# Kernel optimization log

Hardware: AMD Instinct MI355X
Metric: run time of the kernel (lower is better)

The kernel has to match this reference:

```python
import jax, jax.numpy as jnp
import numpy as np

T, B, F = 160, 640, 40          # time-major input [T, B, F]
H, PJ, L = 768, 256, 3          # nb_hidden, nb_proj, nb_layers
FORGET_BIAS = 1.0               # TF LSTMCell default


def _glorot(k, shape):
    std = (2.0 / (shape[0] + shape[1])) ** 0.5
    return jax.random.normal(k, shape, jnp.float32) * std


def setup_inputs() -> dict:
    key = jax.random.key(0)
    ks = jax.random.split(key, 7)
    x = jax.random.normal(ks[0], (T, B, F), jnp.float32)
    # layer 0: input dim F + proj state PJ; layers 1,2: input dim PJ + PJ
    W0 = _glorot(ks[1], (F + PJ, 4 * H)); b0 = jnp.zeros((4 * H,), jnp.float32)
    P0 = _glorot(ks[2], (H, PJ))
    W1 = _glorot(ks[3], (PJ + PJ, 4 * H)); b1 = jnp.zeros((4 * H,), jnp.float32)
    P1 = _glorot(ks[4], (H, PJ))
    W2 = _glorot(ks[5], (PJ + PJ, 4 * H)); b2 = jnp.zeros((4 * H,), jnp.float32)
    P2 = _glorot(ks[6], (H, PJ))
    return {"x": x, "W0": W0, "b0": b0, "P0": P0,
            "W1": W1, "b1": b1, "P1": P1,
            "W2": W2, "b2": b2, "P2": P2}


def _cell(xt, c, h, W, b, P):
    # TF LSTMCell with num_proj: gates on [x, m_prev]; gate order i, j, f, o.
    z = jnp.concatenate([xt, h], axis=-1) @ W + b            # [B, 4H]
    i, j, f, o = jnp.split(z, 4, axis=-1)
    c_new = jax.nn.sigmoid(f + FORGET_BIAS) * c + jax.nn.sigmoid(i) * jnp.tanh(j)
    m = jax.nn.sigmoid(o) * jnp.tanh(c_new)                  # [B, H]
    h_new = m @ P                                            # projected state [B, PJ]
    return c_new, h_new


def reference(x, W0, b0, P0, W1, b1, P1, W2, b2, P2):
    params = ((W0, b0, P0), (W1, b1, P1), (W2, b2, P2))
    Bd = x.shape[1]
    init = tuple((jnp.zeros((Bd, H), x.dtype), jnp.zeros((Bd, PJ), x.dtype))
                 for _ in range(L))

    def step(carry, xt):
        inp = xt
        new = []
        for (c, h), (W, b, P) in zip(carry, params):
            c, h = _cell(inp, c, h, W, b, P)
            new.append((c, h))
            inp = h
        return tuple(new), None

    carry, _ = jax.lax.scan(step, init, x)
    emb = carry[-1][1]                                       # last layer h at final step, [B, PJ]
    # tf.nn.l2_normalize
    return emb / jnp.sqrt(jnp.maximum(jnp.sum(emb * emb, axis=-1, keepdims=True), 1e-12))
```

## Files before the change

kernel.cpp:

```cpp
#include <hip/hip_runtime.h>

#define Bdim 640
#define Hdim 768
#define PJdim 256
#define Tdim 160
#define NSTEP (Tdim + 2)

typedef _Float16 half8 __attribute__((ext_vector_type(8)));
typedef float floatx4 __attribute__((ext_vector_type(4)));

constexpr size_t HB_HALFS = 3ull * Bdim * PJdim;
constexpr size_t ZP_OFF   = HB_HALFS * 2;
constexpr size_t MB_OFF   = ZP_OFF + 256;
constexpr size_t MB_HALFS = 3ull * Bdim * Hdim;
constexpr size_t X_OFF    = MB_OFF + MB_HALFS * 2;
constexpr size_t X_HALFS  = (size_t)Tdim * Bdim * 40;
constexpr size_t W_OFF    = X_OFF + X_HALFS * 2;
constexpr size_t W_HALFS  = 36ull * 131072;
constexpr size_t P_OFF    = W_OFF + W_HALFS * 2;
constexpr size_t P_HALFS  = 3ull * 196608;
constexpr size_t C_OFF    = P_OFF + P_HALFS * 2;
constexpr size_t C_BYTES  = 3ull * Bdim * Hdim * 4;

__device__ __forceinline__ float sigm(float v) { return 1.0f / (1.0f + __expf(-v)); }
__device__ __forceinline__ float tanh_fast(float v) { return 2.0f / (1.0f + __expf(-2.0f * v)) - 1.0f; }

__device__ __forceinline__ void pipe_wait(unsigned* c0, unsigned t0, unsigned* c1, unsigned t1)
{
    if (threadIdx.x == 0) {
        if (t0)
            while (__hip_atomic_load(c0, __ATOMIC_RELAXED, __HIP_MEMORY_SCOPE_AGENT) < t0)
                __builtin_amdgcn_s_sleep(1);
        if (c1 && t1)
            while (__hip_atomic_load(c1, __ATOMIC_RELAXED, __HIP_MEMORY_SCOPE_AGENT) < t1)
                __builtin_amdgcn_s_sleep(1);
        __threadfence();
    }
    __syncthreads();
}

__device__ __forceinline__ void pipe_sig(unsigned* c)
{
    __syncthreads();
    if (threadIdx.x == 0) {
        __threadfence();
        __hip_atomic_fetch_add(c, 1u, __ATOMIC_RELAXED, __HIP_MEMORY_SCOPE_AGENT);
    }
}

__global__ void repack_kernel(const float* __restrict__ x,
                              const float* __restrict__ W0, const float* __restrict__ W1,
                              const float* __restrict__ W2, const float* __restrict__ P0,
                              const float* __restrict__ P1, const float* __restrict__ P2,
                              _Float16* __restrict__ Wfrag, _Float16* __restrict__ Pfrag,
                              _Float16* __restrict__ x16)
{
    size_t idx = (size_t)blockIdx.x * 256 + threadIdx.x;
    if (idx < W_HALFS) {
        int slab = (int)(idx >> 17);
        int l = slab / 12, ht = slab % 12;
        int r  = (int)(idx & 131071);
        int kc = r >> 13;
        int r2 = r & 8191;
        int g  = r2 >> 11;
        int cf = (r2 >> 9) & 3;
        int u  = r2 & 511;
        int lane = u >> 3, e = u & 7;
        int qd = lane >> 4, ln = lane & 15;
        int k   = kc * 32 + qd * 8 + e;
        int col = g * Hdim + ht * 64 + cf * 16 + ln;
        float v;
        if (l == 0)      v = (k < 296) ? W0[(size_t)k * 3072 + col] : 0.0f;
        else if (l == 1) v = W1[(size_t)k * 3072 + col];
        else             v = W2[(size_t)k * 3072 + col];
        Wfrag[idx] = (_Float16)v;
    } else if (idx < W_HALFS + P_HALFS) {
        size_t i = idx - W_HALFS;
        int l = (int)(i / 196608);
        int r = (int)(i % 196608);
        int cq = r / 49152;
        int r2 = r % 49152;
        int kc = r2 / 2048;
        int r3 = r2 & 2047;
        int cgr = r3 >> 9;
        int u  = r3 & 511;
        int lane = u >> 3, e = u & 7;
        int qd = lane >> 4, ln = lane & 15;
        int k  = kc * 32 + qd * 8 + e;
        int pj = cq * 64 + cgr * 16 + ln;
        const float* P = (l == 0) ? P0 : (l == 1) ? P1 : P2;
        Pfrag[i] = (_Float16)P[(size_t)k * PJdim + pj];
    } else if (idx < W_HALFS + P_HALFS + X_HALFS) {
        size_t i = idx - W_HALFS - P_HALFS;
        x16[i] = (_Float16)x[i];
    }
}

__device__ __forceinline__ void gate_step(
    int l, int b0r, int h0, int KC, int t,
    const half8 (&Breg)[16][2], float (&c)[8][2],
    const float (&bia)[2], const float (&bja)[2], const float (&bfa)[2], const float (&boa)[2],
    const _Float16* __restrict__ x16, const _Float16* __restrict__ h16,
    const _Float16* __restrict__ zerop, _Float16* __restrict__ mbuf,
    _Float16* __restrict__ Ast, float* __restrict__ zst, int tid)
{
    const int wv = tid >> 6, lane = tid & 63, qd = lane >> 4, ln = lane & 15;
    const int g = wv >> 1, hh = wv & 1;
    const int qd8 = qd * 8;
    const int rowg = b0r + wv * 16 + ln;

    const _Float16* xt  = x16 + ((size_t)t * Bdim + rowg) * 40;
    const _Float16* h0b = h16 + (size_t)rowg * PJdim - 40;
    const _Float16* lob = (l > 0) ? h16 + ((size_t)(l - 1) * Bdim + rowg) * PJdim : nullptr;
    const _Float16* hib = h16 + ((size_t)l * Bdim + rowg) * PJdim - 256;

    auto srcp = [&](int kc) -> const _Float16* {
        int k = kc * 32 + qd8;
        if (l == 0) return (k < 40) ? xt + k : (k < 296) ? h0b + k : zerop;
        return (k < 256) ? lob + k : hib + k;
    };

    floatx4 acc[8][2];
    const floatx4 fz = {0.f, 0.f, 0.f, 0.f};
#pragma unroll
    for (int i = 0; i < 8; ++i) { acc[i][0] = fz; acc[i][1] = fz; }

    const int CH = KC >> 1;
    uint4 pre0 = *(const uint4*)srcp(0);
    uint4 pre1 = *(const uint4*)srcp(1);
#pragma unroll
    for (int ch = 0; ch < 8; ++ch) {
        if (ch < CH) {
            _Float16* Aw = Ast + (size_t)(ch & 1) * 8192 + wv * 512 + lane * 8;
            *(uint4*)Aw          = pre0;
            *(uint4*)(Aw + 4096) = pre1;
            if (ch + 1 < CH) {
                pre0 = *(const uint4*)srcp(2 * ch + 2);
                pre1 = *(const uint4*)srcp(2 * ch + 3);
            }
            __syncthreads();
            const _Float16* Ab = Ast + (size_t)(ch & 1) * 8192;
#pragma unroll
            for (int sub = 0; sub < 2; ++sub)
#pragma unroll
                for (int rf = 0; rf < 8; ++rf) {
                    half8 af = *(const half8*)(Ab + sub * 4096 + rf * 512 + lane * 8);
                    acc[rf][0] = __builtin_amdgcn_mfma_f32_16x16x32_f16(af, Breg[2 * ch + sub][0], acc[rf][0], 0, 0, 0);
                    acc[rf][1] = __builtin_amdgcn_mfma_f32_16x16x32_f16(af, Breg[2 * ch + sub][1], acc[rf][1], 0, 0, 0);
                }
        }
    }

    const int trow = tid >> 5;
    const int hc0  = (tid * 2) & 63;
#pragma unroll
    for (int rf = 0; rf < 8; ++rf) {
        __syncthreads();
#pragma unroll
        for (int cf = 0; cf < 2; ++cf)
#pragma unroll
            for (int r = 0; r < 4; ++r)
                zst[(qd * 4 + r) * 256 + g * 64 + hh * 32 + cf * 16 + ln] = acc[rf][cf][r];
        __syncthreads();
        _Float16 mh[2];
#pragma unroll
        for (int j = 0; j < 2; ++j) {
            int hc = hc0 + j;
            float zi = zst[trow * 256 + hc]       + bia[j];
            float zj = zst[trow * 256 + 64 + hc]  + bja[j];
            float zf = zst[trow * 256 + 128 + hc] + bfa[j];
            float zo = zst[trow * 256 + 192 + hc] + boa[j];
            float cn = sigm(zf) * c[rf][j] + sigm(zi) * tanh_fast(zj);
            c[rf][j] = cn;
            mh[j] = (_Float16)(sigm(zo) * tanh_fast(cn));
        }
        union { _Float16 h2[2]; unsigned u; } pk;
        pk.h2[0] = mh[0]; pk.h2[1] = mh[1];
        int row_g = b0r + rf * 16 + trow;
        *(unsigned*)(mbuf + ((size_t)l * Bdim + row_g) * Hdim + h0 + hc0) = pk.u;
    }
}

__device__ __forceinline__ void proj_step(
    int l, int b0r, int cq, const half8 (&Preg)[24],
    const _Float16* __restrict__ mbuf, _Float16* __restrict__ h16,
    _Float16* __restrict__ Ast, int tid)
{
    const int wv = tid >> 6, lane = tid & 63, qd = lane >> 4, ln = lane & 15;
    const int rh = wv >> 2, cgi = wv & 3;
    const int rowg = b0r + wv * 16 + ln;
    const _Float16* mrow = mbuf + ((size_t)l * Bdim + rowg) * Hdim + qd * 8;

    floatx4 pacc[4];
    const floatx4 fz = {0.f, 0.f, 0.f, 0.f};
#pragma unroll
    for (int i = 0; i < 4; ++i) pacc[i] = fz;

    uint4 pre0 = *(const uint4*)(mrow);
    uint4 pre1 = *(const uint4*)(mrow + 32);
#pragma unroll
    for (int ch = 0; ch < 12; ++ch) {
        _Float16* Aw = Ast + (size_t)(ch & 1) * 8192 + wv * 512 + lane * 8;
        *(uint4*)Aw          = pre0;
        *(uint4*)(Aw + 4096) = pre1;
        if (ch < 11) {
            pre0 = *(const uint4*)(mrow + (2 * ch + 2) * 32);
            pre1 = *(const uint4*)(mrow + (2 * ch + 3) * 32);
        }
        __syncthreads();
        const _Float16* Ab = Ast + (size_t)(ch & 1) * 8192;
#pragma unroll
        for (int sub = 0; sub < 2; ++sub)
#pragma unroll
            for (int rfl = 0; rfl < 4; ++rfl) {
                half8 af = *(const half8*)(Ab + sub * 4096 + (rh * 4 + rfl) * 512 + lane * 8);
                pacc[rfl] = __builtin_amdgcn_mfma_f32_16x16x32_f16(af, Preg[2 * ch + sub], pacc[rfl], 0, 0, 0);
            }
    }
#pragma unroll
    for (int rfl = 0; rfl < 4; ++rfl)
#pragma unroll
        for (int r = 0; r < 4; ++r) {
            int row = b0r + (rh * 4 + rfl) * 16 + qd * 4 + r;
            h16[((size_t)l * Bdim + row) * PJdim + cq * 64 + cgi * 16 + ln] = (_Float16)pacc[rfl][r];
        }
}

__device__ __forceinline__ void load_Breg(const _Float16* __restrict__ Wfrag, int l, int ht,
                                          int wv, int lane, half8 (&Breg)[16][2])
{
    const int g = wv >> 1, hh = wv & 1;
    const _Float16* wslab = Wfrag + ((size_t)(l * 12 + ht)) * 131072;
#pragma unroll
    for (int kc = 0; kc < 16; ++kc)
#pragma unroll
        for (int cf = 0; cf < 2; ++cf)
            Breg[kc][cf] = *(const half8*)(wslab + kc * 8192 + g * 2048 + (hh * 2 + cf) * 512 + lane * 8);
}

__device__ __forceinline__ void load_Preg(const _Float16* __restrict__ Pfrag, int l, int cq,
                                          int wv, int lane, half8 (&Preg)[24])
{
    const int cgi = wv & 3;
    const _Float16* pslab = Pfrag + (size_t)l * 196608 + (size_t)cq * 49152;
#pragma unroll
    for (int kc = 0; kc < 24; ++kc)
        Preg[kc] = *(const half8*)(pslab + kc * 2048 + cgi * 512 + lane * 8);
}

__device__ __forceinline__ void load_bias(const float* __restrict__ bias, int h0, int tid,
                                          float (&bia)[2], float (&bja)[2], float (&bfa)[2], float (&boa)[2])
{
    int hcg = h0 + ((tid * 2) & 63);
#pragma unroll
    for (int j = 0; j < 2; ++j) {
        bia[j] = bias[hcg + j];
        bja[j] = bias[Hdim + hcg + j];
        bfa[j] = bias[2 * Hdim + hcg + j] + 1.0f;
        boa[j] = bias[3 * Hdim + hcg + j];
    }
}

__device__ __forceinline__ void finalize_row(const _Float16* __restrict__ h16,
                                             float* __restrict__ out, int row, int lane)
{
    const _Float16* e = h16 + ((size_t)2 * Bdim + row) * PJdim + lane * 4;
    float v0 = (float)e[0], v1 = (float)e[1], v2 = (float)e[2], v3 = (float)e[3];
    float ss = v0 * v0 + v1 * v1 + v2 * v2 + v3 * v3;
#pragma unroll
    for (int o = 32; o > 0; o >>= 1) ss += __shfl_xor(ss, o, 64);
    float rs = rsqrtf(fmaxf(ss, 1e-12f));
    float4 o4; o4.x = v0 * rs; o4.y = v1 * rs; o4.z = v2 * rs; o4.w = v3 * rs;
    *(float4*)(out + (size_t)row * PJdim + lane * 4) = o4;
}

__global__ __launch_bounds__(512)
void lstm_persist(const _Float16* __restrict__ x16, const _Float16* __restrict__ Wfrag,
                  const _Float16* __restrict__ Pfrag,
                  const float* __restrict__ bias0, const float* __restrict__ bias1,
                  const float* __restrict__ bias2,
                  _Float16* __restrict__ h16, _Float16* __restrict__ mbuf,
                  const _Float16* __restrict__ zerop, float* __restrict__ out,
                  unsigned* __restrict__ flags)
{
    __shared__ __align__(16) _Float16 Ast[2 * 8192];
    __shared__ __align__(16) float zst[16 * 256];

    const int tid = threadIdx.x, bid = blockIdx.x;
    const int wv = tid >> 6, lane = tid & 63;

    const int xcd = bid & 7, slot = bid >> 3;
    const int gid = xcd * 2 + (slot >> 4);
    const int rr  = slot & 15;
    if (gid >= 15) return;
    const int bt2 = gid / 3, l = gid % 3;
    const int b0r = bt2 * 128;

    unsigned* gd = flags + (size_t)gid * 64;
    unsigned* pd = gd + 32;

    if (rr < 12) {
        const int ht = rr, h0 = ht * 64;
        const int KC = (l == 0) ? 10 : 16;
        half8 Breg[16][2];
        load_Breg(Wfrag, l, ht, wv, lane, Breg);
        float bia[2], bja[2], bfa[2], boa[2];
        load_bias((l == 0) ? bias0 : (l == 1) ? bias1 : bias2, h0, tid, bia, bja, bfa, boa);
        float c[8][2];
#pragma unroll
        for (int i = 0; i < 8; ++i) { c[i][0] = 0.f; c[i][1] = 0.f; }
        unsigned* pd_lo = (l > 0) ? flags + (size_t)(gid - 1) * 64 + 32 : nullptr;
        for (int t = 0; t < Tdim; ++t) {
            pipe_wait(pd, 4u * (unsigned)t, pd_lo, (l > 0) ? 4u * (unsigned)(t + 1) : 0u);
            gate_step(l, b0r, h0, KC, t, Breg, c, bia, bja, bfa, boa,
                      x16, h16, zerop, mbuf, Ast, zst, tid);
            pipe_sig(gd);
        }
        if (l == 2 && rr < 8) {
            pipe_wait(pd, 4u * (unsigned)Tdim, nullptr, 0u);
            int row0 = b0r + rr * 16 + wv * 2;
            finalize_row(h16, out, row0, lane);
            finalize_row(h16, out, row0 + 1, lane);
        }
    } else {
        const int cq = rr - 12;
        half8 Preg[24];
        load_Preg(Pfrag, l, cq, wv, lane, Preg);
        unsigned* gd_hi = (l < 2) ? flags + (size_t)(gid + 1) * 64 : nullptr;
        for (int t = 0; t < Tdim; ++t) {
            pipe_wait(gd, 12u * (unsigned)(t + 1), gd_hi, (l < 2) ? 12u * (unsigned)t : 0u);
            proj_step(l, b0r, cq, Preg, mbuf, h16, Ast, tid);
            pipe_sig(pd);
        }
    }
}

__global__ __launch_bounds__(512)
void gate_fb(const _Float16* __restrict__ x16, const _Float16* __restrict__ Wfrag,
             const float* __restrict__ bias0, const float* __restrict__ bias1,
             const float* __restrict__ bias2,
             _Float16* __restrict__ h16, _Float16* __restrict__ mbuf,
             const _Float16* __restrict__ zerop, float* __restrict__ cfb, int s)
{
    __shared__ __align__(16) _Float16 Ast[2 * 8192];
    __shared__ __align__(16) float zst[16 * 256];
    const int tid = threadIdx.x, bid = blockIdx.x;
    const int ht = bid % 12, z = bid / 12, l = z % 3, bt2 = z / 3;
    const int t = s - l;
    if (t < 0 || t >= Tdim) return;
    const int wv = tid >> 6, lane = tid & 63;
    const int b0r = bt2 * 128, h0 = ht * 64;
    const int KC = (l == 0) ? 10 : 16;
    half8 Breg[16][2];
    load_Breg(Wfrag, l, ht, wv, lane, Breg);
    float bia[2], bja[2], bfa[2], boa[2];
    load_bias((l == 0) ? bias0 : (l == 1) ? bias1 : bias2, h0, tid, bia, bja, bfa, boa);
    const int trow = tid >> 5, hc0 = (tid * 2) & 63;
    float c[8][2];
#pragma unroll
    for (int rf = 0; rf < 8; ++rf)
#pragma unroll
        for (int j = 0; j < 2; ++j)
            c[rf][j] = cfb[((size_t)l * Bdim + b0r + rf * 16 + trow) * Hdim + h0 + hc0 + j];
    gate_step(l, b0r, h0, KC, t, Breg, c, bia, bja, bfa, boa, x16, h16, zerop, mbuf, Ast, zst, tid);
#pragma unroll
    for (int rf = 0; rf < 8; ++rf)
#pragma unroll
        for (int j = 0; j < 2; ++j)
            cfb[((size_t)l * Bdim + b0r + rf * 16 + trow) * Hdim + h0 + hc0 + j] = c[rf][j];
}

__global__ __launch_bounds__(512)
void proj_fb(const _Float16* __restrict__ Pfrag, const _Float16* __restrict__ mbuf,
             _Float16* __restrict__ h16, int s)
{
    __shared__ __align__(16) _Float16 Ast[2 * 8192];
    const int tid = threadIdx.x, bid = blockIdx.x;
    const int cq = bid & 3, z = bid >> 2, l = z % 3, bt2 = z / 3;
    const int tp = s - l;
    if (tp < 0 || tp >= Tdim) return;
    const int wv = tid >> 6, lane = tid & 63;
    half8 Preg[24];
    load_Preg(Pfrag, l, cq, wv, lane, Preg);
    proj_step(l, bt2 * 128, cq, Preg, mbuf, h16, Ast, tid);
}

__global__ __launch_bounds__(512)
void fin_fb(const _Float16* __restrict__ h16, float* __restrict__ out)
{
    int row = blockIdx.x * 8 + (threadIdx.x >> 6);
    finalize_row(h16, out, row, threadIdx.x & 63);
}

extern "C" void kernel_launch(void* const* d_in, const int* in_sizes, int n_in,
                              void* d_out, int out_size, void* d_ws, size_t ws_size,
                              hipStream_t stream)
{
    (void)in_sizes; (void)n_in; (void)out_size; (void)ws_size;
    const float* x  = (const float*)d_in[0];
    const float* W0 = (const float*)d_in[1];
    const float* b0 = (const float*)d_in[2];
    const float* P0 = (const float*)d_in[3];
    const float* W1 = (const float*)d_in[4];
    const float* b1 = (const float*)d_in[5];
    const float* P1 = (const float*)d_in[6];
    const float* W2 = (const float*)d_in[7];
    const float* b2 = (const float*)d_in[8];
    const float* P2 = (const float*)d_in[9];

    char* ws = (char*)d_ws;
    _Float16* h16   = (_Float16*)(ws);
    _Float16* zerop = (_Float16*)(ws + ZP_OFF);
    _Float16* mbuf  = (_Float16*)(ws + MB_OFF);
    _Float16* x16   = (_Float16*)(ws + X_OFF);
    _Float16* Wfrag = (_Float16*)(ws + W_OFF);
    _Float16* Pfrag = (_Float16*)(ws + P_OFF);
    float*    cfb   = (float*)(ws + C_OFF);
    unsigned* flags = (unsigned*)(ws + C_OFF);
    float*    outp  = (float*)d_out;

    hipMemsetAsync(ws, 0, ZP_OFF + 256, stream);
    hipMemsetAsync(cfb, 0, C_BYTES, stream);

    {
        constexpr size_t total = W_HALFS + P_HALFS + X_HALFS;
        int grid = (int)((total + 255) / 256);
        repack_kernel<<<grid, 256, 0, stream>>>(x, W0, W1, W2, P0, P1, P2, Wfrag, Pfrag, x16);
    }

    int occ = 0;
    hipError_t oe = hipOccupancyMaxActiveBlocksPerMultiprocessor(&occ, lstm_persist, 512, 0);
    bool coop = (oe == hipSuccess && occ >= 1);
    if (coop) {
        void* args[] = { (void*)&x16, (void*)&Wfrag, (void*)&Pfrag,
                         (void*)&b0, (void*)&b1, (void*)&b2,
                         (void*)&h16, (void*)&mbuf, (void*)&zerop, (void*)&outp,
                         (void*)&flags };
        hipError_t le = hipLaunchCooperativeKernel((const void*)lstm_persist,
                                                   dim3(256), dim3(512), args, 0, stream);
        if (le != hipSuccess) { (void)hipGetLastError(); coop = false; }
    }
    if (!coop) {
        for (int s = 0; s < NSTEP; ++s) {
            gate_fb<<<180, 512, 0, stream>>>(x16, Wfrag, b0, b1, b2, h16, mbuf, zerop, cfb, s);
            proj_fb<<<60, 512, 0, stream>>>(Pfrag, mbuf, h16, s);
        }
        fin_fb<<<80, 512, 0, stream>>>(h16, outp);
    }
}
```

Measured before the change: 4.839 ms.

## Replace inter-block threadfences with relaxed agent-scope coherent loads and stores

Removes the __threadfence calls from the pipeline wait and signal helpers. All cross-block shared data (h16, mbuf, and the final embedding) is now read and written through relaxed agent-scope atomic loads and stores so that it bypasses non-coherent caches. Launch bounds are also raised to request two blocks per CU. Without fences, the relaxed ordering between the data stores and the flag increment may not guarantee visibility, and the 64-bit split loads and 16-bit atomic stores may be slower than the wide vector accesses they replace.

```diff
diff --git a/kernel.cpp b/kernel.cpp
--- a/kernel.cpp
+++ b/kernel.cpp
@@ -25,6 +25,25 @@
 __device__ __forceinline__ float sigm(float v) { return 1.0f / (1.0f + __expf(-v)); }
 __device__ __forceinline__ float tanh_fast(float v) { return 2.0f / (1.0f + __expf(-2.0f * v)) - 1.0f; }
 
+__device__ __forceinline__ uint4 ld_coh16(const void* p) {
+    const unsigned long long* q = (const unsigned long long*)p;
+    unsigned long long a = __hip_atomic_load(q,     __ATOMIC_RELAXED, __HIP_MEMORY_SCOPE_AGENT);
+    unsigned long long b = __hip_atomic_load(q + 1, __ATOMIC_RELAXED, __HIP_MEMORY_SCOPE_AGENT);
+    uint4 r; r.x = (unsigned)a; r.y = (unsigned)(a >> 32);
+    r.z = (unsigned)b; r.w = (unsigned)(b >> 32);
+    return r;
+}
+__device__ __forceinline__ unsigned long long ld_coh8(const void* p) {
+    return __hip_atomic_load((const unsigned long long*)p, __ATOMIC_RELAXED, __HIP_MEMORY_SCOPE_AGENT);
+}
+__device__ __forceinline__ void st_coh32(void* p, unsigned v) {
+    __hip_atomic_store((unsigned*)p, v, __ATOMIC_RELAXED, __HIP_MEMORY_SCOPE_AGENT);
+}
+__device__ __forceinline__ void st_coh16b(void* p, _Float16 h) {
+    union { _Float16 h; unsigned short u; } cv; cv.h = h;
+    __hip_atomic_store((unsigned short*)p, cv.u, __ATOMIC_RELAXED, __HIP_MEMORY_SCOPE_AGENT);
+}
+
 __device__ __forceinline__ void pipe_wait(unsigned* c0, unsigned t0, unsigned* c1, unsigned t1)
 {
     if (threadIdx.x == 0) {
@@ -34,7 +53,6 @@
         if (c1 && t1)
             while (__hip_atomic_load(c1, __ATOMIC_RELAXED, __HIP_MEMORY_SCOPE_AGENT) < t1)
                 __builtin_amdgcn_s_sleep(1);
-        __threadfence();
     }
     __syncthreads();
 }
@@ -42,10 +60,8 @@
 __device__ __forceinline__ void pipe_sig(unsigned* c)
 {
     __syncthreads();
-    if (threadIdx.x == 0) {
-        __threadfence();
+    if (threadIdx.x == 0)
         __hip_atomic_fetch_add(c, 1u, __ATOMIC_RELAXED, __HIP_MEMORY_SCOPE_AGENT);
-    }
 }
 
 __global__ void repack_kernel(const float* __restrict__ x,
@@ -126,8 +142,8 @@
     for (int i = 0; i < 8; ++i) { acc[i][0] = fz; acc[i][1] = fz; }
 
     const int CH = KC >> 1;
-    uint4 pre0 = *(const uint4*)srcp(0);
-    uint4 pre1 = *(const uint4*)srcp(1);
+    uint4 pre0 = ld_coh16(srcp(0));
+    uint4 pre1 = ld_coh16(srcp(1));
 #pragma unroll
     for (int ch = 0; ch < 8; ++ch) {
         if (ch < CH) {
@@ -135,8 +151,8 @@
             *(uint4*)Aw          = pre0;
             *(uint4*)(Aw + 4096) = pre1;
             if (ch + 1 < CH) {
-                pre0 = *(const uint4*)srcp(2 * ch + 2);
-                pre1 = *(const uint4*)srcp(2 * ch + 3);
+                pre0 = ld_coh16(srcp(2 * ch + 2));
+                pre1 = ld_coh16(srcp(2 * ch + 3));
             }
             __syncthreads();
             const _Float16* Ab = Ast + (size_t)(ch & 1) * 8192;
@@ -177,7 +193,7 @@
         union { _Float16 h2[2]; unsigned u; } pk;
         pk.h2[0] = mh[0]; pk.h2[1] = mh[1];
         int row_g = b0r + rf * 16 + trow;
-        *(unsigned*)(mbuf + ((size_t)l * Bdim + row_g) * Hdim + h0 + hc0) = pk.u;
+        st_coh32(mbuf + ((size_t)l * Bdim + row_g) * Hdim + h0 + hc0, pk.u);
     }
 }
 
@@ -196,16 +212,16 @@
 #pragma unroll
     for (int i = 0; i < 4; ++i) pacc[i] = fz;
 
-    uint4 pre0 = *(const uint4*)(mrow);
-    uint4 pre1 = *(const uint4*)(mrow + 32);
+    uint4 pre0 = ld_coh16(mrow);
+    uint4 pre1 = ld_coh16(mrow + 32);
 #pragma unroll
     for (int ch = 0; ch < 12; ++ch) {
         _Float16* Aw = Ast + (size_t)(ch & 1) * 8192 + wv * 512 + lane * 8;
         *(uint4*)Aw          = pre0;
         *(uint4*)(Aw + 4096) = pre1;
         if (ch < 11) {
-            pre0 = *(const uint4*)(mrow + (2 * ch + 2) * 32);
-            pre1 = *(const uint4*)(mrow + (2 * ch + 3) * 32);
+            pre0 = ld_coh16(mrow + (2 * ch + 2) * 32);
+            pre1 = ld_coh16(mrow + (2 * ch + 3) * 32);
         }
         __syncthreads();
         const _Float16* Ab = Ast + (size_t)(ch & 1) * 8192;
@@ -222,7 +238,8 @@
 #pragma unroll
         for (int r = 0; r < 4; ++r) {
             int row = b0r + (rh * 4 + rfl) * 16 + qd * 4 + r;
-            h16[((size_t)l * Bdim + row) * PJdim + cq * 64 + cgi * 16 + ln] = (_Float16)pacc[rfl][r];
+            st_coh16b(h16 + ((size_t)l * Bdim + row) * PJdim + cq * 64 + cgi * 16 + ln,
+                      (_Float16)pacc[rfl][r]);
         }
 }
 
@@ -265,7 +282,9 @@
                                              float* __restrict__ out, int row, int lane)
 {
     const _Float16* e = h16 + ((size_t)2 * Bdim + row) * PJdim + lane * 4;
-    float v0 = (float)e[0], v1 = (float)e[1], v2 = (float)e[2], v3 = (float)e[3];
+    union { unsigned long long u; _Float16 h[4]; } cv;
+    cv.u = ld_coh8(e);
+    float v0 = (float)cv.h[0], v1 = (float)cv.h[1], v2 = (float)cv.h[2], v3 = (float)cv.h[3];
     float ss = v0 * v0 + v1 * v1 + v2 * v2 + v3 * v3;
 #pragma unroll
     for (int o = 32; o > 0; o >>= 1) ss += __shfl_xor(ss, o, 64);
@@ -274,7 +293,7 @@
     *(float4*)(out + (size_t)row * PJdim + lane * 4) = o4;
 }
 
-__global__ __launch_bounds__(512)
+__global__ __launch_bounds__(512, 2)
 void lstm_persist(const _Float16* __restrict__ x16, const _Float16* __restrict__ Wfrag,
                   const _Float16* __restrict__ Pfrag,
                   const float* __restrict__ bias0, const float* __restrict__ bias1,
@@ -335,7 +354,7 @@
     }
 }
 
-__global__ __launch_bounds__(512)
+__global__ __launch_bounds__(512, 2)
 void gate_fb(const _Float16* __restrict__ x16, const _Float16* __restrict__ Wfrag,
              const float* __restrict__ bias0, const float* __restrict__ bias1,
              const float* __restrict__ bias2,
@@ -370,7 +389,7 @@
             cfb[((size_t)l * Bdim + b0r + rf * 16 + trow) * Hdim + h0 + hc0 + j] = c[rf][j];
 }
 
-__global__ __launch_bounds__(512)
+__global__ __launch_bounds__(512, 2)
 void proj_fb(const _Float16* __restrict__ Pfrag, const _Float16* __restrict__ mbuf,
              _Float16* __restrict__ h16, int s)
 {
```

Result: slower. 5.995 ms (+23.9%).
